# Performance work log

Measured on AMD Instinct MI355X. Metric: run time of the kernel, lower is better.

## Reference

```python
import jax, jax.numpy as jnp
import numpy as np

B, C, N, K = 2, 128, 8192, 16
EPS = 1e-5
SLOPE = 0.2


def _knn_idx(coords, k):
    # coords: [B, 3, N] -> idx: [B, N, k] (k nearest neighbors, self excluded)
    pts = jnp.transpose(coords, (0, 2, 1))            # [B, N, 3]
    sq = jnp.sum(pts * pts, axis=-1)                  # [B, N]
    d2 = sq[:, :, None] + sq[:, None, :] - 2.0 * jnp.einsum('bnd,bmd->bnm', pts, pts)
    _, idx = jax.lax.top_k(-d2, k + 1)                # nearest first; first is self (dist 0)
    return idx[:, :, 1:]


def _graph_feature(feats, idx):
    # feats: [B, C, N], idx: [B, N, k] -> [B, 2C, N, k] = concat(center, neighbor - center)
    gather = jax.vmap(lambda f, i: f[:, i])           # [C,N],[N,k] -> [C,N,k]
    neigh = gather(feats, idx)                        # [B, C, N, k]
    center = jnp.broadcast_to(feats[..., None], neigh.shape)
    return jnp.concatenate([center, neigh - center], axis=1)


def _inorm(x):
    # InstanceNorm2d, affine=False: normalize per (b, c) over spatial dims
    m = jnp.mean(x, axis=(2, 3), keepdims=True)
    v = jnp.var(x, axis=(2, 3), keepdims=True)
    return (x - m) * jax.lax.rsqrt(v + EPS)


def _block(x, W):
    # 1x1 conv (no bias) + instance norm + leaky relu
    y = jnp.einsum('oc,bcnk->bonk', W, x)
    return jax.nn.leaky_relu(_inorm(y), SLOPE)


def setup_inputs() -> dict:
    key = jax.random.key(0)
    k0, k1, k2, k3, k4 = jax.random.split(key, 5)
    coords = jax.random.normal(k0, (B, 3, N), dtype=jnp.float32)
    features = jax.random.normal(k1, (B, C, N), dtype=jnp.float32)
    W1 = jax.random.normal(k2, (C, 2 * C), dtype=jnp.float32) * 0.05
    W2 = jax.random.normal(k3, (2 * C, 2 * C), dtype=jnp.float32) * 0.05
    W3 = jax.random.normal(k4, (C, 4 * C), dtype=jnp.float32) * 0.05
    return {"coords": coords, "features": features, "W1": W1, "W2": W2, "W3": W3}


def reference(coords, features, W1, W2, W3):
    idx = _knn_idx(coords, K)                  # same coords for both gathers -> compute once
    x0 = features                              # [B, C, N]
    x1 = _block(_graph_feature(x0, idx), W1).max(axis=-1)   # [B, C, N]
    x2 = _block(_graph_feature(x1, idx), W2).max(axis=-1)   # [B, 2C, N]
    x3 = jnp.concatenate([x0, x1, x2], axis=1)              # [B, 4C, N]
    y = jnp.einsum('oc,bcn->bon', W3, x3)[..., None]        # [B, C, N, 1]
    out = jax.nn.leaky_relu(_inorm(y), SLOPE)[..., 0]       # [B, C, N]
    return out
```

## Files before the change

### kernel.cpp

```cpp
#include <hip/hip_runtime.h>
#include <math.h>

#define NB 2
#define NPTS 8192
#define CH 128
#define KNN 16
#define K17 17
#define EPSI 1e-5f
#define SLOPE 0.2f
#define NCH 32
#define CHSZ 256
#define SCAP 16
#define BIGF 3.0e38f

#define OFF_IDX   0L
#define OFF_X3    1048576L
#define OFF_UV    34603008L
#define OFF_SURV  OFF_X3
#define OFF_YM    68157440L
#define OFF_CNT   OFF_YM
#define OFF_PA    (OFF_YM + 2097152L)
#define OFF_TAU   (OFF_YM + 10485760L)
#define OFF_WM1   84934656L
#define OFF_WM2   85065728L
#define OFF_STATS 85327872L
#define OFF_PTS4  85336064L


__global__ void zero_stats_k(float* __restrict__ stats) {
  int t = blockIdx.x * 256 + threadIdx.x;
  if (t < 2048) stats[t] = 0.f;
}

__global__ void transpose_x0_k(const float* __restrict__ feat, float* __restrict__ x3) {
  __shared__ float tile[32][33];
  int b = blockIdx.z;
  int n0 = blockIdx.x * 32, c0 = blockIdx.y * 32;
  int tx = threadIdx.x;
  for (int ty = threadIdx.y; ty < 32; ty += 8)
    tile[ty][tx] = feat[((long)b * CH + c0 + ty) * NPTS + n0 + tx];
  __syncthreads();
  for (int ty = threadIdx.y; ty < 32; ty += 8)
    x3[((long)b * NPTS + n0 + ty) * 512 + c0 + tx] = tile[tx][ty];
}

__global__ void prep_w_k(const float* __restrict__ W1, const float* __restrict__ W2,
                         float* __restrict__ Wm1, float* __restrict__ Wm2) {
  int t = blockIdx.x * 256 + threadIdx.x;
  if (t < 256 * 128) {
    int r = t >> 7, k = t & 127;
    Wm1[t] = (r < 128) ? (W1[r * 256 + k] - W1[r * 256 + 128 + k])
                       : W1[(r - 128) * 256 + 128 + k];
  }
  if (t < 512 * 128) {
    int r = t >> 7, k = t & 127;
    Wm2[t] = (r < 256) ? (W2[r * 256 + k] - W2[r * 256 + 128 + k])
                       : W2[(r - 256) * 256 + 128 + k];
  }
}

__global__ void knn_prep_k(const float* __restrict__ coords, float4* __restrict__ pts) {
  int b = blockIdx.y;
  int i = blockIdx.x * 256 + threadIdx.x;
  const float* cb = coords + (long)b * 3 * NPTS;
  float x = cb[i], y = cb[NPTS + i], z = cb[2 * NPTS + i];
  float sq = __fadd_rn(__fadd_rn(__fmul_rn(x, x), __fmul_rn(y, y)), __fmul_rn(z, z));
  pts[(long)b * NPTS + i] = make_float4(x, y, z, sq);
}

#define DIST(pi, pj, d2)                                                          \
  float dot = __fadd_rn(__fadd_rn(__fmul_rn((pi).x, (pj).x), __fmul_rn((pi).y, (pj).y)), \
                        __fmul_rn((pi).z, (pj).z));                               \
  float d2 = __fsub_rn(__fadd_rn((pi).w, (pj).w), __fmul_rn(2.0f, dot));

#define KNN_INSERT(d2v, jv)                                              \
  if ((d2v) < d[K17 - 1]) {                                              \
    _Pragma("unroll")                                                    \
    for (int s = K17 - 1; s > 0; --s) {                                  \
      if ((d2v) < d[s - 1]) { d[s] = d[s - 1]; id[s] = id[s - 1]; }      \
      else if ((d2v) < d[s]) { d[s] = (d2v); id[s] = (jv); }             \
    }                                                                    \
    if ((d2v) < d[0]) { d[0] = (d2v); id[0] = (jv); }                    \
  }

__global__ __launch_bounds__(256) void knn_phaseA_k(const float4* __restrict__ pts,
                                                    float2* __restrict__ pa) {
  int b = blockIdx.y;
  int ib = blockIdx.x & 127;
  int sg = blockIdx.x >> 7;
  int i = ib * 64 + (threadIdx.x & 63);
  int sub = sg * 4 + (threadIdx.x >> 6);
  const float4* P = pts + (long)b * NPTS;
  float4 pi = P[i];
  float d0 = BIGF, d1 = BIGF;
  int i0 = 0x7fffffff, i1 = 0x7fffffff;
  int j0 = sub * 64;
  for (int jj = 0; jj < 64; ++jj) {
    float4 pj = P[j0 + jj];
    DIST(pi, pj, d2)
    if (d2 < d1) {
      if (d2 < d0) { d1 = d0; i1 = i0; d0 = d2; i0 = j0 + jj; }
      else { d1 = d2; i1 = j0 + jj; }
    }
  }
  long base = (((long)b * NPTS + i) * 32 + sub) * 2;
  pa[base] = make_float2(d0, __int_as_float(i0));
  pa[base + 1] = make_float2(d1, __int_as_float(i1));
}

__global__ __launch_bounds__(256) void knn_mergeA_k(const float2* __restrict__ pa,
                                                    float* __restrict__ tau) {
  int b = blockIdx.y;
  int i = blockIdx.x * 256 + threadIdx.x;
  float d[K17]; int id[K17];
#pragma unroll
  for (int s = 0; s < K17; ++s) { d[s] = BIGF; id[s] = 0x7fffffff; }
  long base = ((long)b * NPTS + i) * 64;
  for (int c = 0; c < 64; ++c) {
    float2 v = pa[base + c];
    if (v.x < d[K17 - 1]) {
      int j = __float_as_int(v.y);
      KNN_INSERT(v.x, j);
    }
  }
  tau[(long)b * NPTS + i] = d[K17 - 1];
}

__global__ __launch_bounds__(256) void knn_filter_k(const float4* __restrict__ pts,
                                                    const float* __restrict__ tau,
                                                    float2* __restrict__ surv,
                                                    int* __restrict__ counts) {
  int b = blockIdx.z;
  int i = blockIdx.x * 256 + threadIdx.x;
  int chunk = blockIdx.y;
  const float4* P = pts + (long)b * NPTS;
  float4 pi = P[i];
  float t = tau[(long)b * NPTS + i];
  long sbase = (((long)b * NPTS + i) * NCH + chunk) * SCAP;
  int cnt = 0;
  int j0 = chunk * CHSZ;
#pragma unroll 2
  for (int jj = 0; jj < CHSZ; ++jj) {
    float4 pj = P[j0 + jj];
    DIST(pi, pj, d2)
    if (d2 <= t) {
      if (cnt < SCAP) surv[sbase + cnt] = make_float2(d2, __int_as_float(j0 + jj));
      cnt++;
    }
  }
  counts[((long)b * NPTS + i) * NCH + chunk] = cnt;
}

__global__ __launch_bounds__(256) void knn_mergeB_k(const float2* __restrict__ surv,
                                                    const int* __restrict__ counts,
                                                    const float4* __restrict__ pts,
                                                    int* __restrict__ idxo) {
  __shared__ float2 lds[8][K17][32];
  int b = blockIdx.y;
  int pl = threadIdx.x & 31;
  int sub = threadIdx.x >> 5;
  int i = blockIdx.x * 32 + pl;
  const float4* P = pts + (long)b * NPTS;
  float4 pi = P[i];
  float d[K17]; int id[K17];
#pragma unroll
  for (int s = 0; s < K17; ++s) { d[s] = BIGF; id[s] = 0x7fffffff; }
  long cbase = ((long)b * NPTS + i) * NCH;
  int4 c4 = *(const int4*)(counts + cbase + sub * 4);
  int cnt4[4] = {c4.x, c4.y, c4.z, c4.w};
#pragma unroll
  for (int q = 0; q < 4; ++q) {
    int c = sub * 4 + q;
    int cnt = cnt4[q];
    if (cnt > SCAP) {
      int j0 = c * CHSZ;
      for (int jj = 0; jj < CHSZ; ++jj) {
        float4 pj = P[j0 + jj];
        DIST(pi, pj, d2)
        KNN_INSERT(d2, j0 + jj);
      }
    } else {
      long sb = (cbase + c) * SCAP;
      for (int p = 0; p < cnt; p += 2) {
        float4 v2 = *(const float4*)(surv + sb + p);
        if (v2.x < d[K17 - 1]) {
          int j = __float_as_int(v2.y);
          KNN_INSERT(v2.x, j);
        }
        if (p + 1 < cnt && v2.z < d[K17 - 1]) {
          int j = __float_as_int(v2.w);
          KNN_INSERT(v2.z, j);
        }
      }
    }
  }
#pragma unroll
  for (int s = 0; s < K17; ++s) lds[sub][s][pl] = make_float2(d[s], __int_as_float(id[s]));
  __syncthreads();
  if ((sub & 1) == 0) {
#pragma unroll
    for (int s = 0; s < K17; ++s) {
      float2 v = lds[sub + 1][s][pl];
      if (v.x < d[K17 - 1]) {
        int j = __float_as_int(v.y);
        KNN_INSERT(v.x, j);
      }
    }
  }
  __syncthreads();
  if ((sub & 1) == 0) {
#pragma unroll
    for (int s = 0; s < K17; ++s) lds[sub >> 1][s][pl] = make_float2(d[s], __int_as_float(id[s]));
  }
  __syncthreads();
  if (sub < 2) {
#pragma unroll
    for (int s = 0; s < K17; ++s) {
      float2 v = lds[2 * sub][s][pl];
      d[s] = v.x; id[s] = __float_as_int(v.y);
    }
#pragma unroll
    for (int s = 0; s < K17; ++s) {
      float2 v = lds[2 * sub + 1][s][pl];
      if (v.x < d[K17 - 1]) {
        int j = __float_as_int(v.y);
        KNN_INSERT(v.x, j);
      }
    }
  }
  __syncthreads();
  if (sub < 2) {
#pragma unroll
    for (int s = 0; s < K17; ++s) lds[sub][s][pl] = make_float2(d[s], __int_as_float(id[s]));
  }
  __syncthreads();
  if (sub == 0) {
#pragma unroll
    for (int s = 0; s < K17; ++s) {
      float2 v = lds[0][s][pl];
      d[s] = v.x; id[s] = __float_as_int(v.y);
    }
#pragma unroll
    for (int s = 0; s < K17; ++s) {
      float2 v = lds[1][s][pl];
      if (v.x < d[K17 - 1]) {
        int j = __float_as_int(v.y);
        KNN_INSERT(v.x, j);
      }
    }
    long ob = ((long)b * NPTS + i) * KNN;
#pragma unroll
    for (int s = 1; s < K17; ++s) idxo[ob + s - 1] = id[s];
  }
}

#define GBN 128
#define GBM 64
#define GBK 32
__global__ __launch_bounds__(256) void gemm_xt_k(const float* __restrict__ X, int sx, long xbs,
                                                 const float* __restrict__ W, int K,
                                                 float* __restrict__ Out, int so, long obs) {
  __shared__ float Xs[GBK][GBN + 4];
  __shared__ float Ws[GBK][GBM + 4];
  int b = blockIdx.z;
  const float* Xb = X + (long)b * xbs;
  float* Ob = Out + (long)b * obs;
  int n0 = blockIdx.x * GBN, m0 = blockIdx.y * GBM;
  int tx = threadIdx.x, ty = threadIdx.y;
  int tid = ty * 16 + tx;
  float acc[8][4];
#pragma unroll
  for (int i = 0; i < 8; ++i)
#pragma unroll
    for (int j = 0; j < 4; ++j) acc[i][j] = 0.f;

  for (int k0 = 0; k0 < K; k0 += GBK) {
#pragma unroll
    for (int i = 0; i < 4; ++i) {
      int q = tid + i * 256;
      int r = q >> 3, kq = (q & 7) * 4;
      const float4 v = *(const float4*)(Xb + (long)(n0 + r) * sx + k0 + kq);
      Xs[kq][r] = v.x; Xs[kq + 1][r] = v.y; Xs[kq + 2][r] = v.z; Xs[kq + 3][r] = v.w;
    }
#pragma unroll
    for (int i = 0; i < 2; ++i) {
      int q = tid + i * 256;
      int r = q >> 3, kq = (q & 7) * 4;
      const float4 v = *(const float4*)(W + (long)(m0 + r) * K + k0 + kq);
      Ws[kq][r] = v.x; Ws[kq + 1][r] = v.y; Ws[kq + 2][r] = v.z; Ws[kq + 3][r] = v.w;
    }
    __syncthreads();
#pragma unroll
    for (int kk = 0; kk < GBK; ++kk) {
      float4 w4 = *(const float4*)&Ws[kk][tx * 4];
      float4 xa = *(const float4*)&Xs[kk][ty * 8];
      float4 xb4 = *(const float4*)&Xs[kk][ty * 8 + 4];
      float xs[8] = {xa.x, xa.y, xa.z, xa.w, xb4.x, xb4.y, xb4.z, xb4.w};
      float wv[4] = {w4.x, w4.y, w4.z, w4.w};
#pragma unroll
      for (int i = 0; i < 8; ++i)
#pragma unroll
        for (int j = 0; j < 4; ++j) acc[i][j] = fmaf(xs[i], wv[j], acc[i][j]);
    }
    __syncthreads();
  }
#pragma unroll
  for (int i = 0; i < 8; ++i) {
    float4 v = make_float4(acc[i][0], acc[i][1], acc[i][2], acc[i][3]);
    *(float4*)(Ob + (long)(n0 + ty * 8 + i) * so + m0 + tx * 4) = v;
  }
}

template <int CTILE>
__global__ __launch_bounds__(256) void edge_max_t(const float* __restrict__ uv, int S, int voff,
                                                  int Cout, const int* __restrict__ idx,
                                                  float* __restrict__ ymax,
                                                  float* __restrict__ stats) {
  constexpr int CG = CTILE / 4;
  constexpr int PSL = 256 / CG;
  __shared__ float ls[2][256][4];
  int blk = blockIdx.x;
  int c = (blk & 7) >> 1;
  int b = c >> 1;
  int ct = c & 1;
  int pblk = ((blk >> 3) << 1) | (blk & 1);
  int ch0 = ct * CTILE;
  const float* uvb = uv + (long)b * NPTS * S;
  const int* idxb = idx + (long)b * NPTS * KNN;
  float* ymb = ymax + (long)b * NPTS * Cout;
  int cg = threadIdx.x & (CG - 1);
  int ps = threadIdx.x / CG;
  int n0 = pblk * 32;
  const float* vb = uvb + voff + ch0 + 4 * cg;
  float4 s = make_float4(0.f, 0.f, 0.f, 0.f);
  float4 s2 = make_float4(0.f, 0.f, 0.f, 0.f);
  for (int p = ps; p < 32; p += PSL) {
    int n = n0 + p;
    const int* ip = idxb + n * KNN;
    int4 ia = *(const int4*)(ip);
    int4 ib4 = *(const int4*)(ip + 4);
    int4 ic = *(const int4*)(ip + 8);
    int4 id4 = *(const int4*)(ip + 12);
    int mi[KNN] = {ia.x, ia.y, ia.z, ia.w, ib4.x, ib4.y, ib4.z, ib4.w,
                   ic.x, ic.y, ic.z, ic.w, id4.x, id4.y, id4.z, id4.w};
    float4 u = *(const float4*)(uvb + (long)n * S + ch0 + 4 * cg);
    float4 mx = make_float4(-INFINITY, -INFINITY, -INFINITY, -INFINITY);
#pragma unroll
    for (int k = 0; k < KNN; ++k) {
      float4 v = *(const float4*)(vb + (long)mi[k] * S);
      float4 y;
      y.x = u.x + v.x; y.y = u.y + v.y; y.z = u.z + v.z; y.w = u.w + v.w;
      mx.x = fmaxf(mx.x, y.x); mx.y = fmaxf(mx.y, y.y);
      mx.z = fmaxf(mx.z, y.z); mx.w = fmaxf(mx.w, y.w);
      s.x += y.x; s.y += y.y; s.z += y.z; s.w += y.w;
      s2.x = fmaf(y.x, y.x, s2.x); s2.y = fmaf(y.y, y.y, s2.y);
      s2.z = fmaf(y.z, y.z, s2.z); s2.w = fmaf(y.w, y.w, s2.w);
    }
    *(float4*)(ymb + (long)n * Cout + ch0 + 4 * cg) = mx;
  }
  int t = threadIdx.x;
  ls[0][t][0] = s.x; ls[0][t][1] = s.y; ls[0][t][2] = s.z; ls[0][t][3] = s.w;
  ls[1][t][0] = s2.x; ls[1][t][1] = s2.y; ls[1][t][2] = s2.z; ls[1][t][3] = s2.w;
  __syncthreads();
  if (ps == 0) {
#pragma unroll
    for (int j = 1; j < PSL; ++j) {
      int q = j * CG + cg;
      s.x += ls[0][q][0]; s.y += ls[0][q][1]; s.z += ls[0][q][2]; s.w += ls[0][q][3];
      s2.x += ls[1][q][0]; s2.y += ls[1][q][1]; s2.z += ls[1][q][2]; s2.w += ls[1][q][3];
    }
    float* st = stats + ((long)b * Cout + ch0 + 4 * cg) * 2;
    atomicAdd(&st[0], s.x); atomicAdd(&st[1], s2.x);
    atomicAdd(&st[2], s.y); atomicAdd(&st[3], s2.y);
    atomicAdd(&st[4], s.z); atomicAdd(&st[5], s2.z);
    atomicAdd(&st[6], s.w); atomicAdd(&st[7], s2.w);
  }
}

__global__ void normalize_k(const float* __restrict__ ymax, int Cout,
                            const float* __restrict__ stats, float cinv,
                            float* __restrict__ x3, int coloff) {
  int b = blockIdx.y;
  int o = threadIdx.x & (Cout - 1);
  int n = blockIdx.x * (256 / Cout) + threadIdx.x / Cout;
  const float* st = stats + ((long)b * Cout + o) * 2;
  float mean = st[0] * cinv;
  float var = st[1] * cinv - mean * mean;
  float inv = rsqrtf(var + EPSI);
  float y = ymax[((long)b * NPTS + n) * Cout + o];
  float z = (y - mean) * inv;
  z = z >= 0.f ? z : SLOPE * z;
  x3[((long)b * NPTS + n) * 512 + coloff + o] = z;
}

__global__ void colstats_k(const float* __restrict__ y3, float* __restrict__ stats) {
  int b = blockIdx.y;
  int o = threadIdx.x & 127, slot = threadIdx.x >> 7;
  int n0 = blockIdx.x * 64;
  float s = 0.f, s2 = 0.f;
  for (int p = slot; p < 64; p += 2) {
    float y = y3[((long)b * NPTS + n0 + p) * 128 + o];
    s += y;
    s2 = fmaf(y, y, s2);
  }
  float* st = stats + ((long)b * 128 + o) * 2;
  atomicAdd(&st[0], s);
  atomicAdd(&st[1], s2);
}

__global__ void final_k(const float* __restrict__ y3, const float* __restrict__ stats,
                        float* __restrict__ out) {
  __shared__ float tile[32][33];
  int b = blockIdx.z;
  int n0 = blockIdx.x * 32, o0 = blockIdx.y * 32;
  int tx = threadIdx.x;
  for (int ty = threadIdx.y; ty < 32; ty += 8) {
    int o = o0 + tx;
    const float* st = stats + ((long)b * 128 + o) * 2;
    float mean = st[0] * (1.f / 8192.f);
    float var = st[1] * (1.f / 8192.f) - mean * mean;
    float inv = rsqrtf(var + EPSI);
    float y = y3[((long)b * NPTS + n0 + ty) * 128 + o];
    float z = (y - mean) * inv;
    tile[ty][tx] = z >= 0.f ? z : SLOPE * z;
  }
  __syncthreads();
  for (int ty = threadIdx.y; ty < 32; ty += 8)
    out[((long)b * CH + o0 + ty) * NPTS + n0 + tx] = tile[tx][ty];
}

extern "C" void kernel_launch(void* const* d_in, const int* in_sizes, int n_in,
                              void* d_out, int out_size, void* d_ws, size_t ws_size,
                              hipStream_t stream) {
  const float* coords = (const float*)d_in[0];
  const float* features = (const float*)d_in[1];
  const float* W1 = (const float*)d_in[2];
  const float* W2 = (const float*)d_in[3];
  const float* W3 = (const float*)d_in[4];
  float* out = (float*)d_out;
  char* ws = (char*)d_ws;

  int* idx = (int*)(ws + OFF_IDX);
  float* x3 = (float*)(ws + OFF_X3);
  float* uv = (float*)(ws + OFF_UV);
  float2* surv = (float2*)(ws + OFF_SURV);
  int* counts = (int*)(ws + OFF_CNT);
  float2* pa = (float2*)(ws + OFF_PA);
  float* tau = (float*)(ws + OFF_TAU);
  float* ym = (float*)(ws + OFF_YM);
  float* wm1 = (float*)(ws + OFF_WM1);
  float* wm2 = (float*)(ws + OFF_WM2);
  float* stats = (float*)(ws + OFF_STATS);
  float4* pts4 = (float4*)(ws + OFF_PTS4);

  zero_stats_k<<<8, 256, 0, stream>>>(stats);
  knn_prep_k<<<dim3(NPTS / 256, NB), 256, 0, stream>>>(coords, pts4);
  knn_phaseA_k<<<dim3(1024, NB), 256, 0, stream>>>(pts4, pa);
  knn_mergeA_k<<<dim3(NPTS / 256, NB), 256, 0, stream>>>(pa, tau);
  knn_filter_k<<<dim3(NPTS / 256, NCH, NB), 256, 0, stream>>>(pts4, tau, surv, counts);
  knn_mergeB_k<<<dim3(NPTS / 32, NB), 256, 0, stream>>>(surv, counts, pts4, idx);

  transpose_x0_k<<<dim3(NPTS / 32, CH / 32, NB), dim3(32, 8), 0, stream>>>(features, x3);
  prep_w_k<<<256, 256, 0, stream>>>(W1, W2, wm1, wm2);

  gemm_xt_k<<<dim3(NPTS / GBN, 256 / GBM, NB), dim3(16, 16), 0, stream>>>(
      x3, 512, (long)NPTS * 512, wm1, 128, uv, 256, (long)NPTS * 256);
  edge_max_t<64><<<dim3(NPTS / 32 * 2 * NB), 256, 0, stream>>>(uv, 256, 128, 128, idx, ym, stats);
  normalize_k<<<dim3(NPTS * 128 / 256, NB), 256, 0, stream>>>(ym, 128, stats,
                                                              1.0f / 131072.0f, x3, 128);
  gemm_xt_k<<<dim3(NPTS / GBN, 512 / GBM, NB), dim3(16, 16), 0, stream>>>(
      x3 + 128, 512, (long)NPTS * 512, wm2, 128, uv, 512, (long)NPTS * 512);
  edge_max_t<128><<<dim3(NPTS / 32 * 2 * NB), 256, 0, stream>>>(uv, 512, 256, 256, idx, ym,
                                                                stats + 512);
  normalize_k<<<dim3(NPTS * 256 / 256, NB), 256, 0, stream>>>(ym, 256, stats + 512,
                                                              1.0f / 131072.0f, x3, 256);
  gemm_xt_k<<<dim3(NPTS / GBN, 128 / GBM, NB), dim3(16, 16), 0, stream>>>(
      x3, 512, (long)NPTS * 512, W3, 512, ym, 128, (long)NPTS * 128);
  colstats_k<<<dim3(NPTS / 64, NB), 256, 0, stream>>>(ym, stats + 1536);
  final_k<<<dim3(NPTS / 32, CH / 32, NB), dim3(32, 8), 0, stream>>>(ym, stats + 1536, out);
}
```

Before: 507.9 us.

## Fuse instance-norm and leaky-relu into GEMM loads and final stats into GEMM epilogue

The standalone normalize and colstats passes are removed. Per-channel scale and bias are finalized into a small table, and the normalize plus leaky-relu is applied on the fly as each GEMM loads its input tiles. The last GEMM now reads the three concatenated sources directly instead of a materialized x3 buffer, and it accumulates column sum and sum-of-squares in its epilogue with atomics. Edge-max blocks now cover 16 points instead of 32, which doubles the grid. The intent is to save several full-tensor read/write passes, at the cost of extra ALU work in the GEMM load path and more atomics.

```diff
diff --git a/kernel.cpp b/kernel.cpp
--- a/kernel.cpp
+++ b/kernel.cpp
@@ -14,17 +14,21 @@
 #define BIGF 3.0e38f
 
 #define OFF_IDX   0L
-#define OFF_X3    1048576L
+#define OFF_X0B   1048576L
+#define OFF_YM1   9437184L
+#define OFF_YM2   17825792L
 #define OFF_UV    34603008L
-#define OFF_SURV  OFF_X3
-#define OFF_YM    68157440L
-#define OFF_CNT   OFF_YM
-#define OFF_PA    (OFF_YM + 2097152L)
-#define OFF_TAU   (OFF_YM + 10485760L)
-#define OFF_WM1   84934656L
-#define OFF_WM2   85065728L
-#define OFF_STATS 85327872L
-#define OFF_PTS4  85336064L
+#define OFF_Y4    68157440L
+#define OFF_SURV  OFF_X0B
+#define OFF_PA    OFF_Y4
+#define OFF_CNT   76546048L
+#define OFF_TAU   78643200L
+#define OFF_WM1   78708736L
+#define OFF_WM2   78839808L
+#define OFF_STATS 79101952L
+#define OFF_SCB1  79110144L
+#define OFF_SCB2  79112192L
+#define OFF_PTS4  79116288L
 
 
 __global__ void zero_stats_k(float* __restrict__ stats) {
@@ -32,7 +36,7 @@
   if (t < 2048) stats[t] = 0.f;
 }
 
-__global__ void transpose_x0_k(const float* __restrict__ feat, float* __restrict__ x3) {
+__global__ void transpose_x0_k(const float* __restrict__ feat, float* __restrict__ x0b) {
   __shared__ float tile[32][33];
   int b = blockIdx.z;
   int n0 = blockIdx.x * 32, c0 = blockIdx.y * 32;
@@ -41,7 +45,7 @@
     tile[ty][tx] = feat[((long)b * CH + c0 + ty) * NPTS + n0 + tx];
   __syncthreads();
   for (int ty = threadIdx.y; ty < 32; ty += 8)
-    x3[((long)b * NPTS + n0 + ty) * 512 + c0 + tx] = tile[tx][ty];
+    x0b[((long)b * NPTS + n0 + ty) * 128 + c0 + tx] = tile[tx][ty];
 }
 
 __global__ void prep_w_k(const float* __restrict__ W1, const float* __restrict__ W2,
@@ -56,6 +60,17 @@
     int r = t >> 7, k = t & 127;
     Wm2[t] = (r < 256) ? (W2[r * 256 + k] - W2[r * 256 + 128 + k])
                        : W2[(r - 256) * 256 + 128 + k];
+  }
+}
+
+__global__ void finalize_scb_k(const float* __restrict__ stats, float2* __restrict__ scb,
+                               int count, float cinv) {
+  int t = blockIdx.x * 256 + threadIdx.x;
+  if (t < count) {
+    float mean = stats[t * 2] * cinv;
+    float var = stats[t * 2 + 1] * cinv - mean * mean;
+    float inv = rsqrtf(var + EPSI);
+    scb[t] = make_float2(inv, -mean * inv);
   }
 }
 
@@ -311,7 +326,162 @@
   }
 }
 
-template <int CTILE>
+#define AFFLK4(v, a0, a1, a2, a3)                              \
+  v.x = fmaf(v.x, a0.x, a0.y); v.x = fmaxf(v.x, SLOPE * v.x);  \
+  v.y = fmaf(v.y, a1.x, a1.y); v.y = fmaxf(v.y, SLOPE * v.y);  \
+  v.z = fmaf(v.z, a2.x, a2.y); v.z = fmaxf(v.z, SLOPE * v.z);  \
+  v.w = fmaf(v.w, a3.x, a3.y); v.w = fmaxf(v.w, SLOPE * v.w);
+
+__global__ __launch_bounds__(256) void gemm_aff_k(const float* __restrict__ X,
+                                                  const float2* __restrict__ scb,
+                                                  const float* __restrict__ W,
+                                                  float* __restrict__ Out, int so, long obs) {
+  __shared__ float Xs[GBK][GBN + 4];
+  __shared__ float Ws[GBK][GBM + 4];
+  int b = blockIdx.z;
+  const float* Xb = X + (long)b * NPTS * 128;
+  const float2* sc = scb + b * 128;
+  float* Ob = Out + (long)b * obs;
+  int n0 = blockIdx.x * GBN, m0 = blockIdx.y * GBM;
+  int tx = threadIdx.x, ty = threadIdx.y;
+  int tid = ty * 16 + tx;
+  float acc[8][4];
+#pragma unroll
+  for (int i = 0; i < 8; ++i)
+#pragma unroll
+    for (int j = 0; j < 4; ++j) acc[i][j] = 0.f;
+
+  for (int k0 = 0; k0 < 128; k0 += GBK) {
+#pragma unroll
+    for (int i = 0; i < 4; ++i) {
+      int q = tid + i * 256;
+      int r = q >> 3, kq = (q & 7) * 4;
+      float4 v = *(const float4*)(Xb + (long)(n0 + r) * 128 + k0 + kq);
+      float2 a0 = sc[k0 + kq], a1 = sc[k0 + kq + 1], a2 = sc[k0 + kq + 2], a3 = sc[k0 + kq + 3];
+      AFFLK4(v, a0, a1, a2, a3)
+      Xs[kq][r] = v.x; Xs[kq + 1][r] = v.y; Xs[kq + 2][r] = v.z; Xs[kq + 3][r] = v.w;
+    }
+#pragma unroll
+    for (int i = 0; i < 2; ++i) {
+      int q = tid + i * 256;
+      int r = q >> 3, kq = (q & 7) * 4;
+      const float4 v = *(const float4*)(W + (long)(m0 + r) * 128 + k0 + kq);
+      Ws[kq][r] = v.x; Ws[kq + 1][r] = v.y; Ws[kq + 2][r] = v.z; Ws[kq + 3][r] = v.w;
+    }
+    __syncthreads();
+#pragma unroll
+    for (int kk = 0; kk < GBK; ++kk) {
+      float4 w4 = *(const float4*)&Ws[kk][tx * 4];
+      float4 xa = *(const float4*)&Xs[kk][ty * 8];
+      float4 xb4 = *(const float4*)&Xs[kk][ty * 8 + 4];
+      float xs[8] = {xa.x, xa.y, xa.z, xa.w, xb4.x, xb4.y, xb4.z, xb4.w};
+      float wv[4] = {w4.x, w4.y, w4.z, w4.w};
+#pragma unroll
+      for (int i = 0; i < 8; ++i)
+#pragma unroll
+        for (int j = 0; j < 4; ++j) acc[i][j] = fmaf(xs[i], wv[j], acc[i][j]);
+    }
+    __syncthreads();
+  }
+#pragma unroll
+  for (int i = 0; i < 8; ++i) {
+    float4 v = make_float4(acc[i][0], acc[i][1], acc[i][2], acc[i][3]);
+    *(float4*)(Ob + (long)(n0 + ty * 8 + i) * so + m0 + tx * 4) = v;
+  }
+}
+
+__global__ __launch_bounds__(256) void gemm_cat_k(const float* __restrict__ x0b,
+                                                  const float* __restrict__ ym1,
+                                                  const float* __restrict__ ym2,
+                                                  const float2* __restrict__ scb1,
+                                                  const float2* __restrict__ scb2,
+                                                  const float* __restrict__ W,
+                                                  float* __restrict__ Out,
+                                                  float* __restrict__ st4) {
+  __shared__ float Xs[GBK][GBN + 4];
+  __shared__ float Ws[GBK][GBM + 4];
+  int b = blockIdx.z;
+  float* Ob = Out + (long)b * NPTS * 128;
+  int n0 = blockIdx.x * GBN, m0 = blockIdx.y * GBM;
+  int tx = threadIdx.x, ty = threadIdx.y;
+  int tid = ty * 16 + tx;
+  float acc[8][4];
+#pragma unroll
+  for (int i = 0; i < 8; ++i)
+#pragma unroll
+    for (int j = 0; j < 4; ++j) acc[i][j] = 0.f;
+
+  for (int k0 = 0; k0 < 512; k0 += GBK) {
+    const float* Xb; long st_; const float2* sc_; int cb_;
+    if (k0 < 128)      { Xb = x0b + (long)b * NPTS * 128; st_ = 128; sc_ = nullptr;        cb_ = 0; }
+    else if (k0 < 256) { Xb = ym1 + (long)b * NPTS * 128; st_ = 128; sc_ = scb1 + b * 128; cb_ = 128; }
+    else               { Xb = ym2 + (long)b * NPTS * 256; st_ = 256; sc_ = scb2 + b * 256; cb_ = 256; }
+    int kl = k0 - cb_;
+#pragma unroll
+    for (int i = 0; i < 4; ++i) {
+      int q = tid + i * 256;
+      int r = q >> 3, kq = (q & 7) * 4;
+      float4 v = *(const float4*)(Xb + (long)(n0 + r) * st_ + kl + kq);
+      if (sc_) {
+        float2 a0 = sc_[kl + kq], a1 = sc_[kl + kq + 1], a2 = sc_[kl + kq + 2], a3 = sc_[kl + kq + 3];
+        AFFLK4(v, a0, a1, a2, a3)
+      }
+      Xs[kq][r] = v.x; Xs[kq + 1][r] = v.y; Xs[kq + 2][r] = v.z; Xs[kq + 3][r] = v.w;
+    }
+#pragma unroll
+    for (int i = 0; i < 2; ++i) {
+      int q = tid + i * 256;
+      int r = q >> 3, kq = (q & 7) * 4;
+      const float4 v = *(const float4*)(W + (long)(m0 + r) * 512 + k0 + kq);
+      Ws[kq][r] = v.x; Ws[kq + 1][r] = v.y; Ws[kq + 2][r] = v.z; Ws[kq + 3][r] = v.w;
+    }
+    __syncthreads();
+#pragma unroll
+    for (int kk = 0; kk < GBK; ++kk) {
+      float4 w4 = *(const float4*)&Ws[kk][tx * 4];
+      float4 xa = *(const float4*)&Xs[kk][ty * 8];
+      float4 xb4 = *(const float4*)&Xs[kk][ty * 8 + 4];
+      float xs[8] = {xa.x, xa.y, xa.z, xa.w, xb4.x, xb4.y, xb4.z, xb4.w};
+      float wv[4] = {w4.x, w4.y, w4.z, w4.w};
+#pragma unroll
+      for (int i = 0; i < 8; ++i)
+#pragma unroll
+        for (int j = 0; j < 4; ++j) acc[i][j] = fmaf(xs[i], wv[j], acc[i][j]);
+    }
+    __syncthreads();
+  }
+#pragma unroll
+  for (int i = 0; i < 8; ++i) {
+    float4 v = make_float4(acc[i][0], acc[i][1], acc[i][2], acc[i][3]);
+    *(float4*)(Ob + (long)(n0 + ty * 8 + i) * 128 + m0 + tx * 4) = v;
+  }
+  float cs[4] = {0.f, 0.f, 0.f, 0.f}, cq[4] = {0.f, 0.f, 0.f, 0.f};
+#pragma unroll
+  for (int i = 0; i < 8; ++i)
+#pragma unroll
+    for (int j = 0; j < 4; ++j) { cs[j] += acc[i][j]; cq[j] = fmaf(acc[i][j], acc[i][j], cq[j]); }
+  float* red = (float*)Xs;
+  int base = (tx * 16 + ty) * 8;
+#pragma unroll
+  for (int j = 0; j < 4; ++j) { red[base + 2 * j] = cs[j]; red[base + 2 * j + 1] = cq[j]; }
+  __syncthreads();
+  if (ty == 0) {
+#pragma unroll
+    for (int yy = 1; yy < 16; ++yy) {
+      int bb = (tx * 16 + yy) * 8;
+#pragma unroll
+      for (int j = 0; j < 4; ++j) { cs[j] += red[bb + 2 * j]; cq[j] += red[bb + 2 * j + 1]; }
+    }
+    float* st = st4 + ((long)b * 128 + m0 + tx * 4) * 2;
+#pragma unroll
+    for (int j = 0; j < 4; ++j) {
+      atomicAdd(&st[2 * j], cs[j]);
+      atomicAdd(&st[2 * j + 1], cq[j]);
+    }
+  }
+}
+
+template <int CTILE, int PPB>
 __global__ __launch_bounds__(256) void edge_max_t(const float* __restrict__ uv, int S, int voff,
                                                   int Cout, const int* __restrict__ idx,
                                                   float* __restrict__ ymax,
@@ -330,11 +500,11 @@
   float* ymb = ymax + (long)b * NPTS * Cout;
   int cg = threadIdx.x & (CG - 1);
   int ps = threadIdx.x / CG;
-  int n0 = pblk * 32;
+  int n0 = pblk * PPB;
   const float* vb = uvb + voff + ch0 + 4 * cg;
   float4 s = make_float4(0.f, 0.f, 0.f, 0.f);
   float4 s2 = make_float4(0.f, 0.f, 0.f, 0.f);
-  for (int p = ps; p < 32; p += PSL) {
+  for (int p = ps; p < PPB; p += PSL) {
     int n = n0 + p;
     const int* ip = idxb + n * KNN;
     int4 ia = *(const int4*)(ip);
@@ -375,37 +545,6 @@
     atomicAdd(&st[4], s.z); atomicAdd(&st[5], s2.z);
     atomicAdd(&st[6], s.w); atomicAdd(&st[7], s2.w);
   }
-}
-
-__global__ void normalize_k(const float* __restrict__ ymax, int Cout,
-                            const float* __restrict__ stats, float cinv,
-                            float* __restrict__ x3, int coloff) {
-  int b = blockIdx.y;
-  int o = threadIdx.x & (Cout - 1);
-  int n = blockIdx.x * (256 / Cout) + threadIdx.x / Cout;
-  const float* st = stats + ((long)b * Cout + o) * 2;
-  float mean = st[0] * cinv;
-  float var = st[1] * cinv - mean * mean;
-  float inv = rsqrtf(var + EPSI);
-  float y = ymax[((long)b * NPTS + n) * Cout + o];
-  float z = (y - mean) * inv;
-  z = z >= 0.f ? z : SLOPE * z;
-  x3[((long)b * NPTS + n) * 512 + coloff + o] = z;
-}
-
-__global__ void colstats_k(const float* __restrict__ y3, float* __restrict__ stats) {
-  int b = blockIdx.y;
-  int o = threadIdx.x & 127, slot = threadIdx.x >> 7;
-  int n0 = blockIdx.x * 64;
-  float s = 0.f, s2 = 0.f;
-  for (int p = slot; p < 64; p += 2) {
-    float y = y3[((long)b * NPTS + n0 + p) * 128 + o];
-    s += y;
-    s2 = fmaf(y, y, s2);
-  }
-  float* st = stats + ((long)b * 128 + o) * 2;
-  atomicAdd(&st[0], s);
-  atomicAdd(&st[1], s2);
 }
 
 __global__ void final_k(const float* __restrict__ y3, const float* __restrict__ stats,
@@ -441,16 +580,20 @@
   char* ws = (char*)d_ws;
 
   int* idx = (int*)(ws + OFF_IDX);
-  float* x3 = (float*)(ws + OFF_X3);
+  float* x0b = (float*)(ws + OFF_X0B);
+  float* ym1 = (float*)(ws + OFF_YM1);
+  float* ym2 = (float*)(ws + OFF_YM2);
   float* uv = (float*)(ws + OFF_UV);
+  float* y4 = (float*)(ws + OFF_Y4);
   float2* surv = (float2*)(ws + OFF_SURV);
+  float2* pa = (float2*)(ws + OFF_PA);
   int* counts = (int*)(ws + OFF_CNT);
-  float2* pa = (float2*)(ws + OFF_PA);
   float* tau = (float*)(ws + OFF_TAU);
-  float* ym = (float*)(ws + OFF_YM);
   float* wm1 = (float*)(ws + OFF_WM1);
   float* wm2 = (float*)(ws + OFF_WM2);
   float* stats = (float*)(ws + OFF_STATS);
+  float2* scb1 = (float2*)(ws + OFF_SCB1);
+  float2* scb2 = (float2*)(ws + OFF_SCB2);
   float4* pts4 = (float4*)(ws + OFF_PTS4);
 
   zero_stats_k<<<8, 256, 0, stream>>>(stats);
@@ -460,22 +603,20 @@
   knn_filter_k<<<dim3(NPTS / 256, NCH, NB), 256, 0, stream>>>(pts4, tau, surv, counts);
   knn_mergeB_k<<<dim3(NPTS / 32, NB), 256, 0, stream>>>(surv, counts, pts4, idx);
 
-  transpose_x0_k<<<dim3(NPTS / 32, CH / 32, NB), dim3(32, 8), 0, stream>>>(features, x3);
+  transpose_x0_k<<<dim3(NPTS / 32, CH / 32, NB), dim3(32, 8), 0, stream>>>(features, x0b);
   prep_w_k<<<256, 256, 0, stream>>>(W1, W2, wm1, wm2);
 
   gemm_xt_k<<<dim3(NPTS / GBN, 256 / GBM, NB), dim3(16, 16), 0, stream>>>(
-      x3, 512, (long)NPTS * 512, wm1, 128, uv, 256, (long)NPTS * 256);
-  edge_max_t<64><<<dim3(NPTS / 32 * 2 * NB), 256, 0, stream>>>(uv, 256, 128, 128, idx, ym, stats);
-  normalize_k<<<dim3(NPTS * 128 / 256, NB), 256, 0, stream>>>(ym, 128, stats,
-                                                              1.0f / 131072.0f, x3, 128);
-  gemm_xt_k<<<dim3(NPTS / GBN, 512 / GBM, NB), dim3(16, 16), 0, stream>>>(
-      x3 + 128, 512, (long)NPTS * 512, wm2, 128, uv, 512, (long)NPTS * 512);
-  edge_max_t<128><<<dim3(NPTS / 32 * 2 * NB), 256, 0, stream>>>(uv, 512, 256, 256, idx, ym,
-                                                                stats + 512);
-  normalize_k<<<dim3(NPTS * 256 / 256, NB), 256, 0, stream>>>(ym, 256, stats + 512,
-                                                              1.0f / 131072.0f, x3, 256);
-  gemm_xt_k<<<dim3(NPTS / GBN, 128 / GBM, NB), dim3(16, 16), 0, stream>>>(
-      x3, 512, (long)NPTS * 512, W3, 512, ym, 128, (long)NPTS * 128);
-  colstats_k<<<dim3(NPTS / 64, NB), 256, 0, stream>>>(ym, stats + 1536);
-  final_k<<<dim3(NPTS / 32, CH / 32, NB), dim3(32, 8), 0, stream>>>(ym, stats + 1536, out);
-}
+      x0b, 128, (long)NPTS * 128, wm1, 128, uv, 256, (long)NPTS * 256);
+  edge_max_t<64, 16><<<dim3(NPTS / 16 * 2 * NB), 256, 0, stream>>>(uv, 256, 128, 128, idx,
+                                                                   ym1, stats);
+  finalize_scb_k<<<1, 256, 0, stream>>>(stats, scb1, 256, 1.0f / 131072.0f);
+  gemm_aff_k<<<dim3(NPTS / GBN, 512 / GBM, NB), dim3(16, 16), 0, stream>>>(
+      ym1, scb1, wm2, uv, 512, (long)NPTS * 512);
+  edge_max_t<128, 16><<<dim3(NPTS / 16 * 2 * NB), 256, 0, stream>>>(uv, 512, 256, 256, idx,
+                                                                    ym2, stats + 512);
+  finalize_scb_k<<<2, 256, 0, stream>>>(stats + 512, scb2, 512, 1.0f / 131072.0f);
+  gemm_cat_k<<<dim3(NPTS / GBN, 128 / GBM, NB), dim3(16, 16), 0, stream>>>(
+      x0b, ym1, ym2, scb1, scb2, W3, y4, stats + 1536);
+  final_k<<<dim3(NPTS / 32, CH / 32, NB), dim3(32, 8), 0, stream>>>(y4, stats + 1536, out);
+}
```

Measured after the change: 586.5 us. 15.5% more time.

## Fuse instance-norm and leaky-relu into GEMM input loads, drop concat buffer

Applied to the files above, without the earlier changes.

Removes the separate normalize kernels and the 512-wide x3 concat buffer. Each GEMM now reads the raw max-pooled features, applies a precomputed per-channel scale/bias and leaky relu on the fly, and the final GEMM reads x0, ym1 and ym2 directly. The shared-memory tiled GEMM is replaced by a one-point-per-thread kernel that reads pre-transposed weights with uniform float4 loads. This saves the write and reread of the normalized activations, but gives up LDS reuse of X and may change GEMM efficiency.

```diff
diff --git a/kernel.cpp b/kernel.cpp
--- a/kernel.cpp
+++ b/kernel.cpp
@@ -14,17 +14,22 @@
 #define BIGF 3.0e38f
 
 #define OFF_IDX   0L
-#define OFF_X3    1048576L
+#define OFF_X0B   1048576L
+#define OFF_YM1   9437184L
+#define OFF_YM2   17825792L
 #define OFF_UV    34603008L
-#define OFF_SURV  OFF_X3
-#define OFF_YM    68157440L
-#define OFF_CNT   OFF_YM
-#define OFF_PA    (OFF_YM + 2097152L)
-#define OFF_TAU   (OFF_YM + 10485760L)
-#define OFF_WM1   84934656L
-#define OFF_WM2   85065728L
-#define OFF_STATS 85327872L
-#define OFF_PTS4  85336064L
+#define OFF_Y4    68157440L
+#define OFF_SURV  OFF_X0B
+#define OFF_PA    OFF_Y4
+#define OFF_CNT   76546048L
+#define OFF_TAU   78643200L
+#define OFF_WM1T  78708736L
+#define OFF_WM2T  78839808L
+#define OFF_STATS 79101952L
+#define OFF_SCB1  79110144L
+#define OFF_SCB2  79112192L
+#define OFF_PTS4  79116288L
+#define OFF_W3T   79378432L
 
 
 __global__ void zero_stats_k(float* __restrict__ stats) {
@@ -32,7 +37,7 @@
   if (t < 2048) stats[t] = 0.f;
 }
 
-__global__ void transpose_x0_k(const float* __restrict__ feat, float* __restrict__ x3) {
+__global__ void transpose_x0_k(const float* __restrict__ feat, float* __restrict__ x0b) {
   __shared__ float tile[32][33];
   int b = blockIdx.z;
   int n0 = blockIdx.x * 32, c0 = blockIdx.y * 32;
@@ -41,21 +46,37 @@
     tile[ty][tx] = feat[((long)b * CH + c0 + ty) * NPTS + n0 + tx];
   __syncthreads();
   for (int ty = threadIdx.y; ty < 32; ty += 8)
-    x3[((long)b * NPTS + n0 + ty) * 512 + c0 + tx] = tile[tx][ty];
-}
-
-__global__ void prep_w_k(const float* __restrict__ W1, const float* __restrict__ W2,
-                         float* __restrict__ Wm1, float* __restrict__ Wm2) {
+    x0b[((long)b * NPTS + n0 + ty) * 128 + c0 + tx] = tile[tx][ty];
+}
+
+__global__ void prep_wt_k(const float* __restrict__ W1, const float* __restrict__ W2,
+                          const float* __restrict__ W3, float* __restrict__ Wm1t,
+                          float* __restrict__ Wm2t, float* __restrict__ W3t) {
   int t = blockIdx.x * 256 + threadIdx.x;
-  if (t < 256 * 128) {
-    int r = t >> 7, k = t & 127;
-    Wm1[t] = (r < 128) ? (W1[r * 256 + k] - W1[r * 256 + 128 + k])
-                       : W1[(r - 128) * 256 + 128 + k];
-  }
-  if (t < 512 * 128) {
-    int r = t >> 7, k = t & 127;
-    Wm2[t] = (r < 256) ? (W2[r * 256 + k] - W2[r * 256 + 128 + k])
-                       : W2[(r - 256) * 256 + 128 + k];
+  if (t < 32768) {
+    int k = t >> 8, m = t & 255;
+    Wm1t[t] = (m < 128) ? (W1[m * 256 + k] - W1[m * 256 + 128 + k])
+                        : W1[(m - 128) * 256 + 128 + k];
+  } else if (t < 98304) {
+    int idx = t - 32768;
+    int k = idx >> 9, m = idx & 511;
+    Wm2t[idx] = (m < 256) ? (W2[m * 256 + k] - W2[m * 256 + 128 + k])
+                          : W2[(m - 256) * 256 + 128 + k];
+  } else if (t < 163840) {
+    int idx = t - 98304;
+    int k = idx >> 7, m = idx & 127;
+    W3t[idx] = W3[m * 512 + k];
+  }
+}
+
+__global__ void finalize_scb_k(const float* __restrict__ stats, float2* __restrict__ scb,
+                               int count, float cinv) {
+  int t = blockIdx.x * 256 + threadIdx.x;
+  if (t < count) {
+    float mean = stats[t * 2] * cinv;
+    float var = stats[t * 2 + 1] * cinv - mean * mean;
+    float inv = rsqrtf(var + EPSI);
+    scb[t] = make_float2(inv, -mean * inv);
   }
 }
 
@@ -254,64 +275,117 @@
   }
 }
 
-#define GBN 128
-#define GBM 64
-#define GBK 32
-__global__ __launch_bounds__(256) void gemm_xt_k(const float* __restrict__ X, int sx, long xbs,
-                                                 const float* __restrict__ W, int K,
+#define AFFLK4(v, a0, a1, a2, a3)                              \
+  v.x = fmaf(v.x, a0.x, a0.y); v.x = fmaxf(v.x, SLOPE * v.x);  \
+  v.y = fmaf(v.y, a1.x, a1.y); v.y = fmaxf(v.y, SLOPE * v.y);  \
+  v.z = fmaf(v.z, a2.x, a2.y); v.z = fmaxf(v.z, SLOPE * v.z);  \
+  v.w = fmaf(v.w, a3.x, a3.y); v.w = fmaxf(v.w, SLOPE * v.w);
+
+__device__ __forceinline__ void mac4(float acc[16], float4 xv, const float* __restrict__ wr,
+                                     int M) {
+  float xk[4] = {xv.x, xv.y, xv.z, xv.w};
+#pragma unroll
+  for (int c = 0; c < 4; ++c) {
+    const float4 w0 = *(const float4*)(wr);
+    const float4 w1 = *(const float4*)(wr + 4);
+    const float4 w2 = *(const float4*)(wr + 8);
+    const float4 w3 = *(const float4*)(wr + 12);
+    float x = xk[c];
+    acc[0] = fmaf(x, w0.x, acc[0]);   acc[1] = fmaf(x, w0.y, acc[1]);
+    acc[2] = fmaf(x, w0.z, acc[2]);   acc[3] = fmaf(x, w0.w, acc[3]);
+    acc[4] = fmaf(x, w1.x, acc[4]);   acc[5] = fmaf(x, w1.y, acc[5]);
+    acc[6] = fmaf(x, w1.z, acc[6]);   acc[7] = fmaf(x, w1.w, acc[7]);
+    acc[8] = fmaf(x, w2.x, acc[8]);   acc[9] = fmaf(x, w2.y, acc[9]);
+    acc[10] = fmaf(x, w2.z, acc[10]); acc[11] = fmaf(x, w2.w, acc[11]);
+    acc[12] = fmaf(x, w3.x, acc[12]); acc[13] = fmaf(x, w3.y, acc[13]);
+    acc[14] = fmaf(x, w3.z, acc[14]); acc[15] = fmaf(x, w3.w, acc[15]);
+    wr += M;
+  }
+}
+
+template <bool AFF>
+__global__ __launch_bounds__(256) void gemm_rd_t(const float* __restrict__ X, int sx, long xbs,
+                                                 const float2* __restrict__ scb,
+                                                 const float* __restrict__ Wt, int M, int K,
                                                  float* __restrict__ Out, int so, long obs) {
-  __shared__ float Xs[GBK][GBN + 4];
-  __shared__ float Ws[GBK][GBM + 4];
   int b = blockIdx.z;
-  const float* Xb = X + (long)b * xbs;
-  float* Ob = Out + (long)b * obs;
-  int n0 = blockIdx.x * GBN, m0 = blockIdx.y * GBM;
-  int tx = threadIdx.x, ty = threadIdx.y;
-  int tid = ty * 16 + tx;
-  float acc[8][4];
-#pragma unroll
-  for (int i = 0; i < 8; ++i)
-#pragma unroll
-    for (int j = 0; j < 4; ++j) acc[i][j] = 0.f;
-
-  for (int k0 = 0; k0 < K; k0 += GBK) {
-#pragma unroll
-    for (int i = 0; i < 4; ++i) {
-      int q = tid + i * 256;
-      int r = q >> 3, kq = (q & 7) * 4;
-      const float4 v = *(const float4*)(Xb + (long)(n0 + r) * sx + k0 + kq);
-      Xs[kq][r] = v.x; Xs[kq + 1][r] = v.y; Xs[kq + 2][r] = v.z; Xs[kq + 3][r] = v.w;
-    }
-#pragma unroll
-    for (int i = 0; i < 2; ++i) {
-      int q = tid + i * 256;
-      int r = q >> 3, kq = (q & 7) * 4;
-      const float4 v = *(const float4*)(W + (long)(m0 + r) * K + k0 + kq);
-      Ws[kq][r] = v.x; Ws[kq + 1][r] = v.y; Ws[kq + 2][r] = v.z; Ws[kq + 3][r] = v.w;
-    }
-    __syncthreads();
-#pragma unroll
-    for (int kk = 0; kk < GBK; ++kk) {
-      float4 w4 = *(const float4*)&Ws[kk][tx * 4];
-      float4 xa = *(const float4*)&Xs[kk][ty * 8];
-      float4 xb4 = *(const float4*)&Xs[kk][ty * 8 + 4];
-      float xs[8] = {xa.x, xa.y, xa.z, xa.w, xb4.x, xb4.y, xb4.z, xb4.w};
-      float wv[4] = {w4.x, w4.y, w4.z, w4.w};
-#pragma unroll
-      for (int i = 0; i < 8; ++i)
-#pragma unroll
-        for (int j = 0; j < 4; ++j) acc[i][j] = fmaf(xs[i], wv[j], acc[i][j]);
-    }
-    __syncthreads();
-  }
-#pragma unroll
-  for (int i = 0; i < 8; ++i) {
-    float4 v = make_float4(acc[i][0], acc[i][1], acc[i][2], acc[i][3]);
-    *(float4*)(Ob + (long)(n0 + ty * 8 + i) * so + m0 + tx * 4) = v;
-  }
-}
-
-template <int CTILE>
+  int n = blockIdx.x * 256 + threadIdx.x;
+  int m0 = blockIdx.y * 16;
+  const float* xr = X + (long)b * xbs + (long)n * sx;
+  const float2* sc = AFF ? scb + b * K : nullptr;
+  const float* wp = Wt + m0;
+  float acc[16];
+#pragma unroll
+  for (int j = 0; j < 16; ++j) acc[j] = 0.f;
+#pragma unroll 8
+  for (int k0 = 0; k0 < K; k0 += 4) {
+    float4 xv = *(const float4*)(xr + k0);
+    if (AFF) {
+      float2 a0 = sc[k0], a1 = sc[k0 + 1], a2 = sc[k0 + 2], a3 = sc[k0 + 3];
+      AFFLK4(xv, a0, a1, a2, a3)
+    }
+    mac4(acc, xv, wp + (long)k0 * M, M);
+  }
+  float* ob = Out + (long)b * obs + (long)n * so + m0;
+  *(float4*)(ob) = make_float4(acc[0], acc[1], acc[2], acc[3]);
+  *(float4*)(ob + 4) = make_float4(acc[4], acc[5], acc[6], acc[7]);
+  *(float4*)(ob + 8) = make_float4(acc[8], acc[9], acc[10], acc[11]);
+  *(float4*)(ob + 12) = make_float4(acc[12], acc[13], acc[14], acc[15]);
+}
+
+__global__ __launch_bounds__(256) void gemm_rdcat_k(const float* __restrict__ x0b,
+                                                    const float* __restrict__ ym1,
+                                                    const float* __restrict__ ym2,
+                                                    const float2* __restrict__ scb1,
+                                                    const float2* __restrict__ scb2,
+                                                    const float* __restrict__ Wt,
+                                                    float* __restrict__ Out) {
+  int b = blockIdx.z;
+  int n = blockIdx.x * 256 + threadIdx.x;
+  int m0 = blockIdx.y * 16;
+  long nb = (long)b * NPTS + n;
+  const float* wp = Wt + m0;
+  float acc[16];
+#pragma unroll
+  for (int j = 0; j < 16; ++j) acc[j] = 0.f;
+  {
+    const float* xr = x0b + nb * 128;
+#pragma unroll 8
+    for (int k0 = 0; k0 < 128; k0 += 4) {
+      float4 xv = *(const float4*)(xr + k0);
+      mac4(acc, xv, wp + (long)k0 * 128, 128);
+    }
+  }
+  {
+    const float* xr = ym1 + nb * 128;
+    const float2* sc = scb1 + b * 128;
+#pragma unroll 8
+    for (int k0 = 0; k0 < 128; k0 += 4) {
+      float4 xv = *(const float4*)(xr + k0);
+      float2 a0 = sc[k0], a1 = sc[k0 + 1], a2 = sc[k0 + 2], a3 = sc[k0 + 3];
+      AFFLK4(xv, a0, a1, a2, a3)
+      mac4(acc, xv, wp + (long)(128 + k0) * 128, 128);
+    }
+  }
+  {
+    const float* xr = ym2 + nb * 256;
+    const float2* sc = scb2 + b * 256;
+#pragma unroll 8
+    for (int k0 = 0; k0 < 256; k0 += 4) {
+      float4 xv = *(const float4*)(xr + k0);
+      float2 a0 = sc[k0], a1 = sc[k0 + 1], a2 = sc[k0 + 2], a3 = sc[k0 + 3];
+      AFFLK4(xv, a0, a1, a2, a3)
+      mac4(acc, xv, wp + (long)(256 + k0) * 128, 128);
+    }
+  }
+  float* ob = Out + nb * 128 + m0;
+  *(float4*)(ob) = make_float4(acc[0], acc[1], acc[2], acc[3]);
+  *(float4*)(ob + 4) = make_float4(acc[4], acc[5], acc[6], acc[7]);
+  *(float4*)(ob + 8) = make_float4(acc[8], acc[9], acc[10], acc[11]);
+  *(float4*)(ob + 12) = make_float4(acc[12], acc[13], acc[14], acc[15]);
+}
+
+template <int CTILE, int PPB>
 __global__ __launch_bounds__(256) void edge_max_t(const float* __restrict__ uv, int S, int voff,
                                                   int Cout, const int* __restrict__ idx,
                                                   float* __restrict__ ymax,
@@ -330,11 +404,11 @@
   float* ymb = ymax + (long)b * NPTS * Cout;
   int cg = threadIdx.x & (CG - 1);
   int ps = threadIdx.x / CG;
-  int n0 = pblk * 32;
+  int n0 = pblk * PPB;
   const float* vb = uvb + voff + ch0 + 4 * cg;
   float4 s = make_float4(0.f, 0.f, 0.f, 0.f);
   float4 s2 = make_float4(0.f, 0.f, 0.f, 0.f);
-  for (int p = ps; p < 32; p += PSL) {
+  for (int p = ps; p < PPB; p += PSL) {
     int n = n0 + p;
     const int* ip = idxb + n * KNN;
     int4 ia = *(const int4*)(ip);
@@ -375,22 +449,6 @@
     atomicAdd(&st[4], s.z); atomicAdd(&st[5], s2.z);
     atomicAdd(&st[6], s.w); atomicAdd(&st[7], s2.w);
   }
-}
-
-__global__ void normalize_k(const float* __restrict__ ymax, int Cout,
-                            const float* __restrict__ stats, float cinv,
-                            float* __restrict__ x3, int coloff) {
-  int b = blockIdx.y;
-  int o = threadIdx.x & (Cout - 1);
-  int n = blockIdx.x * (256 / Cout) + threadIdx.x / Cout;
-  const float* st = stats + ((long)b * Cout + o) * 2;
-  float mean = st[0] * cinv;
-  float var = st[1] * cinv - mean * mean;
-  float inv = rsqrtf(var + EPSI);
-  float y = ymax[((long)b * NPTS + n) * Cout + o];
-  float z = (y - mean) * inv;
-  z = z >= 0.f ? z : SLOPE * z;
-  x3[((long)b * NPTS + n) * 512 + coloff + o] = z;
 }
 
 __global__ void colstats_k(const float* __restrict__ y3, float* __restrict__ stats) {
@@ -441,16 +499,21 @@
   char* ws = (char*)d_ws;
 
   int* idx = (int*)(ws + OFF_IDX);
-  float* x3 = (float*)(ws + OFF_X3);
+  float* x0b = (float*)(ws + OFF_X0B);
+  float* ym1 = (float*)(ws + OFF_YM1);
+  float* ym2 = (float*)(ws + OFF_YM2);
   float* uv = (float*)(ws + OFF_UV);
+  float* y4 = (float*)(ws + OFF_Y4);
   float2* surv = (float2*)(ws + OFF_SURV);
+  float2* pa = (float2*)(ws + OFF_PA);
   int* counts = (int*)(ws + OFF_CNT);
-  float2* pa = (float2*)(ws + OFF_PA);
   float* tau = (float*)(ws + OFF_TAU);
-  float* ym = (float*)(ws + OFF_YM);
-  float* wm1 = (float*)(ws + OFF_WM1);
-  float* wm2 = (float*)(ws + OFF_WM2);
+  float* wm1t = (float*)(ws + OFF_WM1T);
+  float* wm2t = (float*)(ws + OFF_WM2T);
+  float* w3t = (float*)(ws + OFF_W3T);
   float* stats = (float*)(ws + OFF_STATS);
+  float2* scb1 = (float2*)(ws + OFF_SCB1);
+  float2* scb2 = (float2*)(ws + OFF_SCB2);
   float4* pts4 = (float4*)(ws + OFF_PTS4);
 
   zero_stats_k<<<8, 256, 0, stream>>>(stats);
@@ -460,22 +523,21 @@
   knn_filter_k<<<dim3(NPTS / 256, NCH, NB), 256, 0, stream>>>(pts4, tau, surv, counts);
   knn_mergeB_k<<<dim3(NPTS / 32, NB), 256, 0, stream>>>(surv, counts, pts4, idx);
 
-  transpose_x0_k<<<dim3(NPTS / 32, CH / 32, NB), dim3(32, 8), 0, stream>>>(features, x3);
-  prep_w_k<<<256, 256, 0, stream>>>(W1, W2, wm1, wm2);
-
-  gemm_xt_k<<<dim3(NPTS / GBN, 256 / GBM, NB), dim3(16, 16), 0, stream>>>(
-      x3, 512, (long)NPTS * 512, wm1, 128, uv, 256, (long)NPTS * 256);
-  edge_max_t<64><<<dim3(NPTS / 32 * 2 * NB), 256, 0, stream>>>(uv, 256, 128, 128, idx, ym, stats);
-  normalize_k<<<dim3(NPTS * 128 / 256, NB), 256, 0, stream>>>(ym, 128, stats,
-                                                              1.0f / 131072.0f, x3, 128);
-  gemm_xt_k<<<dim3(NPTS / GBN, 512 / GBM, NB), dim3(16, 16), 0, stream>>>(
-      x3 + 128, 512, (long)NPTS * 512, wm2, 128, uv, 512, (long)NPTS * 512);
-  edge_max_t<128><<<dim3(NPTS / 32 * 2 * NB), 256, 0, stream>>>(uv, 512, 256, 256, idx, ym,
-                                                                stats + 512);
-  normalize_k<<<dim3(NPTS * 256 / 256, NB), 256, 0, stream>>>(ym, 256, stats + 512,
-                                                              1.0f / 131072.0f, x3, 256);
-  gemm_xt_k<<<dim3(NPTS / GBN, 128 / GBM, NB), dim3(16, 16), 0, stream>>>(
-      x3, 512, (long)NPTS * 512, W3, 512, ym, 128, (long)NPTS * 128);
-  colstats_k<<<dim3(NPTS / 64, NB), 256, 0, stream>>>(ym, stats + 1536);
-  final_k<<<dim3(NPTS / 32, CH / 32, NB), dim3(32, 8), 0, stream>>>(ym, stats + 1536, out);
-}
+  transpose_x0_k<<<dim3(NPTS / 32, CH / 32, NB), dim3(32, 8), 0, stream>>>(features, x0b);
+  prep_wt_k<<<640, 256, 0, stream>>>(W1, W2, W3, wm1t, wm2t, w3t);
+
+  gemm_rd_t<false><<<dim3(NPTS / 256, 16, NB), 256, 0, stream>>>(
+      x0b, 128, (long)NPTS * 128, nullptr, wm1t, 256, 128, uv, 256, (long)NPTS * 256);
+  edge_max_t<64, 32><<<dim3(NPTS / 32 * 2 * NB), 256, 0, stream>>>(uv, 256, 128, 128, idx,
+                                                                   ym1, stats);
+  finalize_scb_k<<<1, 256, 0, stream>>>(stats, scb1, 256, 1.0f / 131072.0f);
+  gemm_rd_t<true><<<dim3(NPTS / 256, 32, NB), 256, 0, stream>>>(
+      ym1, 128, (long)NPTS * 128, scb1, wm2t, 512, 128, uv, 512, (long)NPTS * 512);
+  edge_max_t<128, 32><<<dim3(NPTS / 32 * 2 * NB), 256, 0, stream>>>(uv, 512, 256, 256, idx,
+                                                                    ym2, stats + 512);
+  finalize_scb_k<<<2, 256, 0, stream>>>(stats + 512, scb2, 512, 1.0f / 131072.0f);
+  gemm_rdcat_k<<<dim3(NPTS / 256, 8, NB), 256, 0, stream>>>(x0b, ym1, ym2, scb1, scb2, w3t,
+                                                            y4);
+  colstats_k<<<dim3(NPTS / 64, NB), 256, 0, stream>>>(y4, stats + 1536);
+  final_k<<<dim3(NPTS / 32, CH / 32, NB), dim3(32, 8), 0, stream>>>(y4, stats + 1536, out);
+}
```

Result: slower. 532.5 us (+4.8%).
